# Kernel tuning notes

Measured on AMD Instinct MI355X. Metric: run time of the kernel, lower is better.

The kernel has to match this reference:

```python
import jax, jax.numpy as jnp
import numpy as np

B, Hn, Wn, C, NH, WS, SR = 4, 64, 64, 256, 8, 3, 8
HD = C // NH
N = Hn * Wn
L = WS * WS
PH, PW = Hn // SR, Wn // SR
P = PH * PW
T = 4096  # cpb table length
NEG = -1e30

def _l2norm(x, axis=-1):
    return x / jnp.maximum(jnp.linalg.norm(x, axis=axis, keepdims=True), 1e-12)

def _unfold(x, ws):
    # x: (B, C, H, W) -> (B, C, ws*ws, H*W), torch F.unfold channel ordering (C major)
    p = ws // 2
    b, c, h, w = x.shape
    xp = jnp.pad(x, ((0, 0), (0, 0), (p, p), (p, p)))
    pats = jnp.stack([xp[:, :, i:i + h, j:j + w] for i in range(ws) for j in range(ws)], axis=2)
    return pats.reshape(b, c, ws * ws, h * w)

def setup_inputs():
    key = jax.random.key(0)
    ks = jax.random.split(key, 16)
    def w(k, shape, s=0.02):
        return jax.random.normal(k, shape, jnp.float32) * s
    # buffers derived from the window geometry (get_seqlen_and_mask)
    ones = np.ones((Hn, Wn), np.float32)
    pad = WS // 2
    op = np.pad(ones, pad)
    pats = np.stack([op[i:i + Hn, j:j + Wn] for i in range(WS) for j in range(WS)], -1).reshape(N, L)
    padding_mask = jnp.asarray(pats == 0)
    seq_length_scale = jnp.asarray(np.log(pats.sum(-1, keepdims=True) + P).astype(np.float32))
    temperature = jnp.log(jnp.expm1(jnp.ones((NH, 1, 1), jnp.float32) / 0.24))
    return dict(
        x=jax.random.normal(ks[0], (B, N, C), jnp.float32),
        relative_pos_index=jax.random.randint(ks[1], (N, P), 0, T),
        relative_coords_table=jax.random.uniform(ks[2], (T, 2), jnp.float32, -1.0, 1.0),
        q_w=w(ks[3], (C, C)), q_b=jnp.zeros((C,), jnp.float32),
        kv_w=w(ks[4], (2 * C, C)), kv_b=jnp.zeros((2 * C,), jnp.float32),
        temperature=temperature,
        query_embedding=w(ks[5], (NH, 1, HD)),
        proj_w=w(ks[6], (C, C)), proj_b=jnp.zeros((C,), jnp.float32),
        sr_w=w(ks[7], (C, C)), sr_b=jnp.zeros((C,), jnp.float32),
        norm_g=jnp.ones((C,), jnp.float32), norm_b=jnp.zeros((C,), jnp.float32),
        cpb1_w=w(ks[8], (512, 2)), cpb1_b=jnp.zeros((512,), jnp.float32),
        cpb2_w=w(ks[9], (NH, 512)), cpb2_b=jnp.zeros((NH,), jnp.float32),
        rpb_local=w(ks[10], (NH, L), 0.0004),
        learnable_tokens=w(ks[11], (NH, HD, L)),
        learnable_bias=jnp.zeros((NH, 1, L), jnp.float32),
        seq_length_scale=seq_length_scale,
        padding_mask=padding_mask,
        H=Hn, W=Wn,
    )

def _forward(x, q_w, q_b, kv_w, kv_b, temperature, query_embedding, proj_w, proj_b,
             sr_w, sr_b, norm_g, norm_b, cpb1_w, cpb1_b, cpb2_w, cpb2_b, rpb_local,
             learnable_tokens, learnable_bias, seq_length_scale, relative_coords_table,
             relative_pos_index, padding_mask, H, W):
    b, n, c = x.shape
    # normalized queries, scaled by learnable temperature and log-seqlen
    q = (x @ q_w.T + q_b).reshape(b, n, NH, HD).transpose(0, 2, 1, 3)  # (B,h,N,d)
    q_norm = _l2norm(q)
    q_scaled = (q_norm + query_embedding[None]) * jax.nn.softplus(temperature)[None] * seq_length_scale
    # --- local branch: sliding-window QK with RPB ---
    kv = x @ kv_w.T + kv_b  # (B,N,2C)
    k_loc = _l2norm((kv[..., :c]).reshape(b, n, NH, HD)).reshape(b, n, c)
    kv_img = jnp.concatenate([k_loc, kv[..., c:]], -1).transpose(0, 2, 1).reshape(b, 2 * c, H, W)
    pats = _unfold(kv_img, WS).reshape(b, 2 * NH, HD, L, n).transpose(0, 1, 4, 2, 3)  # (B,2h,N,d,L)
    k_loc, v_loc = pats[:, :NH], pats[:, NH:]
    attn_local = jnp.einsum('bhnd,bhndl->bhnl', q_scaled, k_loc) + rpb_local[None, :, None, :]
    attn_local = jnp.where(padding_mask[None, None], NEG, attn_local)
    # --- pooled branch ---
    x_img = x.transpose(0, 2, 1).reshape(b, c, H, W)
    x_sr = jax.nn.gelu(jnp.einsum('bchw,oc->bohw', x_img, sr_w) + sr_b[None, :, None, None], approximate=False)
    x_pool = x_sr.reshape(b, c, PH, SR, PW, SR).mean((3, 5)).reshape(b, c, P).transpose(0, 2, 1)  # (B,P,C)
    mu = x_pool.mean(-1, keepdims=True)
    var = x_pool.var(-1, keepdims=True)
    x_pool = (x_pool - mu) / jnp.sqrt(var + 1e-5) * norm_g + norm_b
    kv_pool = (x_pool @ kv_w.T + kv_b).reshape(b, P, 2 * NH, HD).transpose(0, 2, 1, 3)
    k_pool, v_pool = kv_pool[:, :NH], kv_pool[:, NH:]  # (B,h,P,d)
    cpb = jax.nn.relu(relative_coords_table @ cpb1_w.T + cpb1_b) @ cpb2_w.T + cpb2_b  # (T,h)
    pool_bias = cpb.T[:, relative_pos_index.reshape(-1)].reshape(NH, n, P)
    attn_pool = jnp.einsum('bhnd,bhpd->bhnp', q_scaled, _l2norm(k_pool)) + pool_bias[None]
    # --- joint softmax over local + pooled keys ---
    attn = jax.nn.softmax(jnp.concatenate([attn_local, attn_pool], -1), axis=-1)
    attn_local, attn_pool = attn[..., :L], attn[..., L:]
    a = jnp.einsum('bhnd,hdl->bhnl', q_norm, learnable_tokens) + learnable_bias[None] + attn_local
    x_local = jnp.einsum('bhnl,bhndl->bhnd', a, v_loc)
    x_pool_out = jnp.einsum('bhnp,bhpd->bhnd', attn_pool, v_pool)
    out = (x_local + x_pool_out).transpose(0, 2, 1, 3).reshape(b, n, c)
    return out @ proj_w.T + proj_b

def reference(x, relative_pos_index, relative_coords_table, q_w, q_b, kv_w, kv_b, temperature,
              query_embedding, proj_w, proj_b, sr_w, sr_b, norm_g, norm_b, cpb1_w, cpb1_b,
              cpb2_w, cpb2_b, rpb_local, learnable_tokens, learnable_bias, seq_length_scale,
              padding_mask, H, W):
    return _forward(x, q_w, q_b, kv_w, kv_b, temperature, query_embedding, proj_w, proj_b,
                    sr_w, sr_b, norm_g, norm_b, cpb1_w, cpb1_b, cpb2_w, cpb2_b, rpb_local,
                    learnable_tokens, learnable_bias, seq_length_scale, relative_coords_table,
                    relative_pos_index, padding_mask, H, W)
```

## Files before the change

### kernel.cpp

```cpp
#include <hip/hip_runtime.h>
#include <hip/hip_bf16.h>

typedef unsigned short u16;
typedef unsigned int u32;

#define B_ 4
#define N_ 4096
#define C_ 256
#define NH_ 8
#define HD_ 32
#define L_ 9
#define P_ 64
#define T_ 4096
#define NEG_ (-1e30f)

typedef __attribute__((ext_vector_type(8))) short bf16x8;
typedef __attribute__((ext_vector_type(4))) float f32x4;

__device__ __forceinline__ float b2f(u16 u) {
    union { u32 i; float f; } v; v.i = ((u32)u) << 16; return v.f;
}
__device__ __forceinline__ u16 f2b(float f) {
    u32 x = __float_as_uint(f);
    u32 r = (x + 0x7fffu + ((x >> 16) & 1u)) >> 16;
    return (u16)r;
}
__device__ __forceinline__ short f2bs(float f) { return (short)f2b(f); }

__global__ __launch_bounds__(256) void prep_k(
    const float* __restrict__ x, const float* __restrict__ q_w, const float* __restrict__ kv_w,
    const float* __restrict__ sr_w, const float* __restrict__ proj_w,
    u16* __restrict__ xb, u16* __restrict__ wfused, u16* __restrict__ pwb,
    const float* __restrict__ table, const float* __restrict__ w1, const float* __restrict__ b1,
    const float* __restrict__ w2, const float* __restrict__ b2, float* __restrict__ cpb)
{
    __shared__ float w1s[512][2];
    __shared__ float b1s[512];
    __shared__ float w2s[8][512];
    int bid = blockIdx.x, tid = threadIdx.x;
    if (bid < 4096) {
        int i = bid * 256 + tid;
        float4 v = reinterpret_cast<const float4*>(x)[i];
        ushort4 o; o.x = f2b(v.x); o.y = f2b(v.y); o.z = f2b(v.z); o.w = f2b(v.w);
        reinterpret_cast<ushort4*>(xb)[i] = o;
    } else if (bid < 4416) {
        int i = (bid - 4096) * 256 + tid;
        const float* s; u16* d; int off;
        if (i < 16384)      { s = q_w;    d = wfused; off = i; }
        else if (i < 49152) { s = kv_w;   d = wfused; off = i; }
        else if (i < 65536) { s = sr_w;   d = wfused; off = i; }
        else                { s = proj_w; d = pwb;    off = i - 65536; }
        int soff = (i < 16384) ? i : (i < 49152) ? (i - 16384) : (i < 65536) ? (i - 49152) : (i - 65536);
        float4 v = reinterpret_cast<const float4*>(s)[soff];
        ushort4 o; o.x = f2b(v.x); o.y = f2b(v.y); o.z = f2b(v.z); o.w = f2b(v.w);
        reinterpret_cast<ushort4*>(d)[off] = o;
    } else {
        for (int i = tid; i < 512; i += 256) {
            w1s[i][0] = w1[i * 2]; w1s[i][1] = w1[i * 2 + 1]; b1s[i] = b1[i];
        }
        for (int i = tid; i < 4096; i += 256) w2s[i >> 9][i & 511] = w2[i];
        __syncthreads();
        int t = (bid - 4416) * 256 + tid;
        float t0 = table[t * 2], t1 = table[t * 2 + 1];
        float acc[8] = {};
        for (int j = 0; j < 512; ++j) {
            float h = fmaxf(t0 * w1s[j][0] + t1 * w1s[j][1] + b1s[j], 0.0f);
            #pragma unroll
            for (int hh = 0; hh < 8; ++hh) acc[hh] += h * w2s[hh][j];
        }
        #pragma unroll
        for (int hh = 0; hh < 8; ++hh) cpb[t * 8 + hh] = acc[hh] + b2[hh];
    }
}

template<int MODE>
__global__ __launch_bounds__(256) void gemm_big_k(
    const u16* __restrict__ A, const u16* __restrict__ W,
    const float* __restrict__ b0, const float* __restrict__ b1, const float* __restrict__ b2,
    float* __restrict__ qn, float* __restrict__ kv, u16* __restrict__ xgb, float* __restrict__ pout)
{
    const int K = 256;
    int tid = threadIdx.x, w = tid >> 6, lane = tid & 63;
    int quad = lane >> 4, l16 = lane & 15;
    int wr = w >> 1, wc = w & 1;
    int rowBase = blockIdx.y * 128 + wr * 64;
    int colBase = blockIdx.x * 128 + wc * 64;
    f32x4 acc[4][4] = {};
    const u16* aptr = A + (size_t)(rowBase + l16) * K + quad * 8;
    const u16* wptr = W + (size_t)(colBase + l16) * K + quad * 8;
    for (int k0 = 0; k0 < K; k0 += 32) {
        bf16x8 af[4], bfr[4];
        #pragma unroll
        for (int i = 0; i < 4; ++i) af[i] = *reinterpret_cast<const bf16x8*>(aptr + (size_t)i * 16 * K + k0);
        #pragma unroll
        for (int j = 0; j < 4; ++j) bfr[j] = *reinterpret_cast<const bf16x8*>(wptr + (size_t)j * 16 * K + k0);
        #pragma unroll
        for (int i = 0; i < 4; ++i)
            #pragma unroll
            for (int j = 0; j < 4; ++j)
                acc[i][j] = __builtin_amdgcn_mfma_f32_16x16x32_bf16(af[i], bfr[j], acc[i][j], 0, 0, 0);
    }
    int rng = (MODE == 0) ? (colBase >> 8) : 99;
    float bj[4];
    #pragma unroll
    for (int j = 0; j < 4; ++j) {
        int gc = colBase + j * 16 + l16;
        if (MODE == 1)      bj[j] = b0[gc];
        else if (rng == 0)  bj[j] = b0[gc];
        else if (rng <= 2)  bj[j] = b1[gc - 256];
        else                bj[j] = b2[gc - 768];
    }
    #pragma unroll
    for (int i = 0; i < 4; ++i) {
        float vals[4][4];
        #pragma unroll
        for (int j = 0; j < 4; ++j)
            #pragma unroll
            for (int r = 0; r < 4; ++r) {
                float t = acc[i][j][r] + bj[j];
                if (MODE == 0 && rng == 3) t = 0.5f * t * (1.0f + erff(t * 0.70710678118654752f));
                vals[j][r] = t;
            }
        if (MODE == 0 && rng <= 1) {
            #pragma unroll
            for (int hp = 0; hp < 2; ++hp)
                #pragma unroll
                for (int r = 0; r < 4; ++r) {
                    float s = vals[2*hp][r] * vals[2*hp][r] + vals[2*hp+1][r] * vals[2*hp+1][r];
                    s += __shfl_xor(s, 1); s += __shfl_xor(s, 2);
                    s += __shfl_xor(s, 4); s += __shfl_xor(s, 8);
                    float inv = 1.0f / fmaxf(sqrtf(s), 1e-12f);
                    vals[2*hp][r] *= inv; vals[2*hp+1][r] *= inv;
                }
        }
        #pragma unroll
        for (int j = 0; j < 4; ++j) {
            int gc = colBase + j * 16 + l16;
            #pragma unroll
            for (int r = 0; r < 4; ++r) {
                int row = rowBase + i * 16 + quad * 4 + r;
                if (MODE == 1)      pout[(size_t)row * 256 + gc] = vals[j][r];
                else if (rng == 0)  qn[(size_t)row * 256 + gc] = vals[j][r];
                else if (rng <= 2)  kv[(size_t)row * 512 + gc - 256] = vals[j][r];
                else                xgb[(size_t)row * 256 + gc - 768] = f2b(vals[j][r]);
            }
        }
    }
}

__global__ __launch_bounds__(256) void poolkv_k(
    const u16* __restrict__ xgb, const float* __restrict__ g, const float* __restrict__ bta,
    const float* __restrict__ kv_w, const float* __restrict__ kv_b, float* __restrict__ kvp)
{
    __shared__ __align__(16) float xps[256];
    __shared__ float r1[4], r2[4];
    int bp = blockIdx.x;
    int b = bp >> 6, p = bp & 63;
    int py = p >> 3, px = p & 7;
    int o = threadIdx.x;
    float s = 0.0f;
    for (int sy = 0; sy < 8; ++sy)
        #pragma unroll
        for (int sx = 0; sx < 8; ++sx) {
            int pix = (py * 8 + sy) * 64 + px * 8 + sx;
            s += b2f(xgb[((size_t)(b * N_ + pix)) * C_ + o]);
        }
    float v = s * (1.0f / 64.0f);
    float s1 = v, s2 = v * v;
    #pragma unroll
    for (int off = 32; off >= 1; off >>= 1) { s1 += __shfl_xor(s1, off); s2 += __shfl_xor(s2, off); }
    int wv = o >> 6, ln = o & 63;
    if (ln == 0) { r1[wv] = s1; r2[wv] = s2; }
    __syncthreads();
    float S1 = r1[0] + r1[1] + r1[2] + r1[3];
    float S2 = r2[0] + r2[1] + r2[2] + r2[3];
    float mu = S1 * (1.0f / 256.0f);
    float var = S2 * (1.0f / 256.0f) - mu * mu;
    xps[o] = (v - mu) * rsqrtf(var + 1e-5f) * g[o] + bta[o];
    __syncthreads();
    float a0 = kv_b[o], a1 = kv_b[o + 256];
    const float4* xp4 = (const float4*)xps;
    const float4* w0 = (const float4*)(kv_w + (size_t)o * 256);
    const float4* w1 = (const float4*)(kv_w + (size_t)(o + 256) * 256);
    #pragma unroll 4
    for (int k4 = 0; k4 < 64; ++k4) {
        float4 xv = xp4[k4]; float4 wa = w0[k4]; float4 wb = w1[k4];
        a0 += xv.x * wa.x + xv.y * wa.y + xv.z * wa.z + xv.w * wa.w;
        a1 += xv.x * wb.x + xv.y * wb.y + xv.z * wb.z + xv.w * wb.w;
    }
    float ss = a0 * a0;
    ss += __shfl_xor(ss, 1); ss += __shfl_xor(ss, 2); ss += __shfl_xor(ss, 4);
    ss += __shfl_xor(ss, 8); ss += __shfl_xor(ss, 16);
    a0 *= 1.0f / fmaxf(sqrtf(ss), 1e-12f);
    kvp[(size_t)bp * 512 + o] = a0;
    kvp[(size_t)bp * 512 + 256 + o] = a1;
}

__global__ __launch_bounds__(256) void attn_k(
    const float* __restrict__ qn, const float* __restrict__ kv,
    const float* __restrict__ kvp, const float* __restrict__ cpb,
    const int* __restrict__ rpi, const float* __restrict__ temp,
    const float* __restrict__ qe, const float* __restrict__ lt,
    const float* __restrict__ rpb, const float* __restrict__ lb,
    const float* __restrict__ slsin, u16* __restrict__ aob)
{
    __shared__ u16 kp_hi[64 * 40], kp_lo[64 * 40];
    __shared__ u16 vp_hi[32 * 72], vp_lo[32 * 72];
    __shared__ u16 ltb[16 * 32];
    __shared__ float qs_w[4][16][36];
    __shared__ float S_w[4][16][88];
    __shared__ float rpb_s[9], lb_s[9];

    int bid = blockIdx.x;
    int tile = bid & 63, h = (bid >> 6) & 7, b = bid >> 9;
    int tid = threadIdx.x, wave = tid >> 6, lane = tid & 63;
    int quad = lane >> 4, l16 = lane & 15;

    {
        int p = tid >> 2, dc = (tid & 3) * 8;
        const float* src = kvp + ((size_t)(b * P_ + p)) * 512 + h * 32 + dc;
        float4 k0 = *(const float4*)(src), k1 = *(const float4*)(src + 4);
        float4 v0 = *(const float4*)(src + 256), v1 = *(const float4*)(src + 260);
        float kf[8] = {k0.x,k0.y,k0.z,k0.w,k1.x,k1.y,k1.z,k1.w};
        float vf[8] = {v0.x,v0.y,v0.z,v0.w,v1.x,v1.y,v1.z,v1.w};
        #pragma unroll
        for (int j = 0; j < 8; ++j) {
            u16 khi = f2b(kf[j]);
            kp_hi[p * 40 + dc + j] = khi;
            kp_lo[p * 40 + dc + j] = f2b(kf[j] - b2f(khi));
            u16 vhi = f2b(vf[j]);
            vp_hi[(dc + j) * 72 + p] = vhi;
            vp_lo[(dc + j) * 72 + p] = f2b(vf[j] - b2f(vhi));
        }
    }
    for (int t = tid; t < 512; t += 256) {
        int l = t & 15, d = t >> 4;
        ltb[l * 32 + d] = (l < 9) ? f2b(lt[h * 288 + d * 9 + l]) : (u16)0;
    }
    if (tid < 9) { rpb_s[tid] = rpb[h * 9 + tid]; lb_s[tid] = lb[h * 9 + tid]; }
    __syncthreads();

    int n0w = tile * 64 + wave * 16;
    float tsc = log1pf(expf(temp[h]));
    bf16x8 qs_hi, qs_lo, qn_b;
    {
        int n = n0w + l16;
        const float* qptr = qn + ((size_t)(b * N_ + n)) * C_ + h * 32 + quad * 8;
        float4 q0 = *(const float4*)qptr, q1 = *(const float4*)(qptr + 4);
        const float* qeptr = qe + h * 32 + quad * 8;
        float4 e0 = *(const float4*)qeptr, e1 = *(const float4*)(qeptr + 4);
        float slv = slsin[n];
        float qf[8] = {q0.x,q0.y,q0.z,q0.w,q1.x,q1.y,q1.z,q1.w};
        float ef[8] = {e0.x,e0.y,e0.z,e0.w,e1.x,e1.y,e1.z,e1.w};
        #pragma unroll
        for (int j = 0; j < 8; ++j) {
            float qs = (qf[j] + ef[j]) * tsc * slv;
            u16 hi = f2b(qs);
            qs_hi[j] = (short)hi;
            qs_lo[j] = f2bs(qs - b2f(hi));
            qn_b[j]  = f2bs(qf[j]);
            qs_w[wave][l16][quad * 8 + j] = qs;
        }
        if (quad == 0) { S_w[wave][l16][73] = NEG_; S_w[wave][l16][74] = NEG_; S_w[wave][l16][75] = NEG_; }
    }

    #pragma unroll
    for (int jt = 0; jt < 4; ++jt) {
        bf16x8 bh = *(const bf16x8*)&kp_hi[(jt * 16 + l16) * 40 + quad * 8];
        bf16x8 bl = *(const bf16x8*)&kp_lo[(jt * 16 + l16) * 40 + quad * 8];
        f32x4 a = {};
        a = __builtin_amdgcn_mfma_f32_16x16x32_bf16(qs_lo, bh, a, 0, 0, 0);
        a = __builtin_amdgcn_mfma_f32_16x16x32_bf16(qs_hi, bl, a, 0, 0, 0);
        a = __builtin_amdgcn_mfma_f32_16x16x32_bf16(qs_hi, bh, a, 0, 0, 0);
        #pragma unroll
        for (int r = 0; r < 4; ++r) {
            int pix = quad * 4 + r;
            int n = n0w + pix;
            int idx = rpi[n * P_ + jt * 16 + l16];
            S_w[wave][pix][jt * 16 + l16] = a[r] + cpb[(size_t)idx * 8 + h];
        }
    }
    f32x4 accL;
    {
        bf16x8 ltf = *(const bf16x8*)&ltb[l16 * 32 + quad * 8];
        f32x4 z = {};
        accL = __builtin_amdgcn_mfma_f32_16x16x32_bf16(qn_b, ltf, z, 0, 0, 0);
    }
    for (int t = lane; t < 144; t += 64) {
        int pix = t / 9, l = t - pix * 9;
        int n = n0w + pix, y = n >> 6, x = n & 63;
        int ny = y + l / 3 - 1, nx = x + (l % 3) - 1;
        bool ok = ((unsigned)ny < 64u) && ((unsigned)nx < 64u);
        int nn = ok ? ny * 64 + nx : n;
        const float4* kb = (const float4*)(kv + ((size_t)(b * N_ + nn)) * 512 + h * 32);
        float acl = 0.0f;
        #pragma unroll
        for (int d4 = 0; d4 < 8; ++d4) {
            float4 kk = kb[d4];
            float4 qq = *(const float4*)&qs_w[wave][pix][d4 * 4];
            acl += qq.x * kk.x + qq.y * kk.y + qq.z * kk.z + qq.w * kk.w;
        }
        S_w[wave][pix][64 + l] = ok ? (acl + rpb_s[l]) : NEG_;
    }
    {
        int pix = lane >> 2, c0 = (lane & 3) * 19;
        float vals[19]; float mx = NEG_;
        #pragma unroll
        for (int i = 0; i < 19; ++i) { vals[i] = S_w[wave][pix][c0 + i]; mx = fmaxf(mx, vals[i]); }
        mx = fmaxf(mx, __shfl_xor(mx, 1));
        mx = fmaxf(mx, __shfl_xor(mx, 2));
        float sm = 0.0f;
        #pragma unroll
        for (int i = 0; i < 19; ++i) { vals[i] = expf(vals[i] - mx); sm += vals[i]; }
        sm += __shfl_xor(sm, 1); sm += __shfl_xor(sm, 2);
        float inv = 1.0f / sm;
        #pragma unroll
        for (int i = 0; i < 19; ++i) S_w[wave][pix][c0 + i] = vals[i] * inv;
    }
    if (l16 < 9) {
        #pragma unroll
        for (int r = 0; r < 4; ++r) {
            int pix = quad * 4 + r;
            int n = n0w + pix, y = n >> 6, x = n & 63;
            int ny = y + l16 / 3 - 1, nx = x + (l16 % 3) - 1;
            bool ok = ((unsigned)ny < 64u) && ((unsigned)nx < 64u);
            S_w[wave][pix][76 + l16] = ok ? (accL[r] + lb_s[l16] + S_w[wave][pix][64 + l16]) : 0.0f;
        }
    }
    f32x4 accO[2] = {};
    #pragma unroll
    for (int kc = 0; kc < 2; ++kc) {
        float wf[8];
        *(float4*)&wf[0] = *(const float4*)&S_w[wave][l16][kc * 32 + quad * 8];
        *(float4*)&wf[4] = *(const float4*)&S_w[wave][l16][kc * 32 + quad * 8 + 4];
        bf16x8 w_hi, w_lo;
        #pragma unroll
        for (int j = 0; j < 8; ++j) {
            u16 hi = f2b(wf[j]);
            w_hi[j] = (short)hi;
            w_lo[j] = f2bs(wf[j] - b2f(hi));
        }
        #pragma unroll
        for (int nt = 0; nt < 2; ++nt) {
            bf16x8 vh = *(const bf16x8*)&vp_hi[(nt * 16 + l16) * 72 + kc * 32 + quad * 8];
            bf16x8 vl = *(const bf16x8*)&vp_lo[(nt * 16 + l16) * 72 + kc * 32 + quad * 8];
            accO[nt] = __builtin_amdgcn_mfma_f32_16x16x32_bf16(w_lo, vh, accO[nt], 0, 0, 0);
            accO[nt] = __builtin_amdgcn_mfma_f32_16x16x32_bf16(w_hi, vl, accO[nt], 0, 0, 0);
            accO[nt] = __builtin_amdgcn_mfma_f32_16x16x32_bf16(w_hi, vh, accO[nt], 0, 0, 0);
        }
    }
    #pragma unroll
    for (int r = 0; r < 4; ++r) {
        int pix = quad * 4 + r;
        int n = n0w + pix, y = n >> 6, x = n & 63;
        #pragma unroll
        for (int l = 0; l < 9; ++l) {
            int ny = y + l / 3 - 1, nx = x + (l % 3) - 1;
            bool ok = ((unsigned)ny < 64u) && ((unsigned)nx < 64u);
            int nn = ok ? ny * 64 + nx : n;
            float aw = S_w[wave][pix][76 + l];
            const float* vb = kv + ((size_t)(b * N_ + nn)) * 512 + 256 + h * 32;
            accO[0][r] += aw * vb[l16];
            accO[1][r] += aw * vb[16 + l16];
        }
    }
    #pragma unroll
    for (int nt = 0; nt < 2; ++nt)
        #pragma unroll
        for (int r = 0; r < 4; ++r) {
            int n = n0w + quad * 4 + r;
            aob[((size_t)(b * N_ + n)) * C_ + h * 32 + nt * 16 + l16] = f2b(accO[nt][r]);
        }
}

extern "C" void kernel_launch(void* const* d_in, const int* in_sizes, int n_in,
                              void* d_out, int out_size, void* d_ws, size_t ws_size,
                              hipStream_t stream) {
    const float* x      = (const float*)d_in[0];
    const int*   rpi    = (const int*)d_in[1];
    const float* table  = (const float*)d_in[2];
    const float* q_w    = (const float*)d_in[3];
    const float* q_b    = (const float*)d_in[4];
    const float* kv_w   = (const float*)d_in[5];
    const float* kv_b   = (const float*)d_in[6];
    const float* temp   = (const float*)d_in[7];
    const float* qe     = (const float*)d_in[8];
    const float* proj_w = (const float*)d_in[9];
    const float* proj_b = (const float*)d_in[10];
    const float* sr_w   = (const float*)d_in[11];
    const float* sr_b   = (const float*)d_in[12];
    const float* norm_g = (const float*)d_in[13];
    const float* norm_b = (const float*)d_in[14];
    const float* cpb1_w = (const float*)d_in[15];
    const float* cpb1_b = (const float*)d_in[16];
    const float* cpb2_w = (const float*)d_in[17];
    const float* cpb2_b = (const float*)d_in[18];
    const float* rpb    = (const float*)d_in[19];
    const float* lt     = (const float*)d_in[20];
    const float* lb     = (const float*)d_in[21];
    const float* sls    = (const float*)d_in[22];

    float* ws  = (float*)d_ws;
    float* qn  = ws;
    float* kv  = qn  + (size_t)B_ * N_ * C_;
    float* kvp = kv  + (size_t)B_ * N_ * 2 * C_;
    float* cpb = kvp + (size_t)B_ * P_ * 2 * C_;
    u16*   xb  = (u16*)(cpb + (size_t)T_ * NH_);
    u16*   wfb = xb  + (size_t)B_ * N_ * C_;
    u16*   pwb = wfb + (size_t)1024 * C_;
    u16*   xgb = pwb + (size_t)C_ * C_;
    u16*   aob = xgb;

    dim3 blk(256);

    prep_k<<<dim3(4432), blk, 0, stream>>>(x, q_w, kv_w, sr_w, proj_w, xb, wfb, pwb,
                                           table, cpb1_w, cpb1_b, cpb2_w, cpb2_b, cpb);
    gemm_big_k<0><<<dim3(8, 128), blk, 0, stream>>>(xb, wfb, q_b, kv_b, sr_b, qn, kv, xgb, nullptr);
    poolkv_k<<<dim3(B_ * P_), blk, 0, stream>>>(xgb, norm_g, norm_b, kv_w, kv_b, kvp);
    attn_k<<<dim3(B_ * NH_ * 64), blk, 0, stream>>>(qn, kv, kvp, cpb, rpi, temp, qe, lt, rpb, lb, sls, aob);
    gemm_big_k<1><<<dim3(2, 128), blk, 0, stream>>>(aob, pwb, proj_b, nullptr, nullptr,
                                                    nullptr, nullptr, nullptr, (float*)d_out);
}
```

Baseline: 293.9 us.

## Stage weight tiles in LDS for GEMMs, split pooled KV projection across blocks

The GEMM kernel now loads a 64-column slab of the full-K weight matrix into shared memory once per block. Each wave computes RI×4 MFMA tiles against that slab, with 64 columns per block and a grid reshaped to 16×64 and 4×256. The pooled KV kernel doubles its block count so each block computes only K or only V, which halves the per-thread dot-product work. The attention kernel moves its local weights to a separate small shared array and hoists the temperature computation ahead of the barrier. The GEMM change trades some A-matrix register reuse and more blocks for less global weight traffic.

New measurement: 277.4 us. 1.06x faster.

```diff
diff --git a/kernel.cpp b/kernel.cpp
--- a/kernel.cpp
+++ b/kernel.cpp
@@ -79,26 +79,35 @@
     const float* __restrict__ b0, const float* __restrict__ b1, const float* __restrict__ b2,
     float* __restrict__ qn, float* __restrict__ kv, u16* __restrict__ xgb, float* __restrict__ pout)
 {
-    const int K = 256;
+    constexpr int RI = (MODE == 0) ? 4 : 1;
+    __shared__ u16 Bs[64 * 264];
     int tid = threadIdx.x, w = tid >> 6, lane = tid & 63;
     int quad = lane >> 4, l16 = lane & 15;
-    int wr = w >> 1, wc = w & 1;
-    int rowBase = blockIdx.y * 128 + wr * 64;
-    int colBase = blockIdx.x * 128 + wc * 64;
-    f32x4 acc[4][4] = {};
-    const u16* aptr = A + (size_t)(rowBase + l16) * K + quad * 8;
-    const u16* wptr = W + (size_t)(colBase + l16) * K + quad * 8;
-    for (int k0 = 0; k0 < K; k0 += 32) {
-        bf16x8 af[4], bfr[4];
-        #pragma unroll
-        for (int i = 0; i < 4; ++i) af[i] = *reinterpret_cast<const bf16x8*>(aptr + (size_t)i * 16 * K + k0);
-        #pragma unroll
-        for (int j = 0; j < 4; ++j) bfr[j] = *reinterpret_cast<const bf16x8*>(wptr + (size_t)j * 16 * K + k0);
-        #pragma unroll
-        for (int i = 0; i < 4; ++i)
+    int colBase = blockIdx.x * 64;
+    #pragma unroll
+    for (int c = 0; c < 8; ++c) {
+        int linear = c * 256 + tid;
+        int col = linear >> 5, kc = linear & 31;
+        uint4 v = *reinterpret_cast<const uint4*>(W + (size_t)(colBase + col) * 256 + kc * 8);
+        *reinterpret_cast<uint4*>(&Bs[col * 264 + kc * 8]) = v;
+    }
+    __syncthreads();
+    int rowBase = blockIdx.y * (RI * 64) + w * (RI * 16);
+    f32x4 acc[RI][4] = {};
+    const u16* aptr = A + (size_t)(rowBase + l16) * 256 + quad * 8;
+    #pragma unroll
+    for (int k0 = 0; k0 < 256; k0 += 32) {
+        bf16x8 af[RI];
+        #pragma unroll
+        for (int i = 0; i < RI; ++i)
+            af[i] = *reinterpret_cast<const bf16x8*>(aptr + (size_t)i * 16 * 256 + k0);
+        #pragma unroll
+        for (int j = 0; j < 4; ++j) {
+            bf16x8 bfr = *reinterpret_cast<const bf16x8*>(&Bs[(j * 16 + l16) * 264 + k0 + quad * 8]);
             #pragma unroll
-            for (int j = 0; j < 4; ++j)
-                acc[i][j] = __builtin_amdgcn_mfma_f32_16x16x32_bf16(af[i], bfr[j], acc[i][j], 0, 0, 0);
+            for (int i = 0; i < RI; ++i)
+                acc[i][j] = __builtin_amdgcn_mfma_f32_16x16x32_bf16(af[i], bfr, acc[i][j], 0, 0, 0);
+        }
     }
     int rng = (MODE == 0) ? (colBase >> 8) : 99;
     float bj[4];
@@ -111,7 +120,7 @@
         else                bj[j] = b2[gc - 768];
     }
     #pragma unroll
-    for (int i = 0; i < 4; ++i) {
+    for (int i = 0; i < RI; ++i) {
         float vals[4][4];
         #pragma unroll
         for (int j = 0; j < 4; ++j)
@@ -154,7 +163,8 @@
 {
     __shared__ __align__(16) float xps[256];
     __shared__ float r1[4], r2[4];
-    int bp = blockIdx.x;
+    int bid = blockIdx.x;
+    int bp = bid >> 1, half = bid & 1;
     int b = bp >> 6, p = bp & 63;
     int py = p >> 3, px = p & 7;
     int o = threadIdx.x;
@@ -178,22 +188,22 @@
     float var = S2 * (1.0f / 256.0f) - mu * mu;
     xps[o] = (v - mu) * rsqrtf(var + 1e-5f) * g[o] + bta[o];
     __syncthreads();
-    float a0 = kv_b[o], a1 = kv_b[o + 256];
+    int col = half * 256 + o;
+    float a = kv_b[col];
     const float4* xp4 = (const float4*)xps;
-    const float4* w0 = (const float4*)(kv_w + (size_t)o * 256);
-    const float4* w1 = (const float4*)(kv_w + (size_t)(o + 256) * 256);
-    #pragma unroll 4
+    const float4* wrow = (const float4*)(kv_w + (size_t)col * 256);
+    #pragma unroll 8
     for (int k4 = 0; k4 < 64; ++k4) {
-        float4 xv = xp4[k4]; float4 wa = w0[k4]; float4 wb = w1[k4];
-        a0 += xv.x * wa.x + xv.y * wa.y + xv.z * wa.z + xv.w * wa.w;
-        a1 += xv.x * wb.x + xv.y * wb.y + xv.z * wb.z + xv.w * wb.w;
-    }
-    float ss = a0 * a0;
-    ss += __shfl_xor(ss, 1); ss += __shfl_xor(ss, 2); ss += __shfl_xor(ss, 4);
-    ss += __shfl_xor(ss, 8); ss += __shfl_xor(ss, 16);
-    a0 *= 1.0f / fmaxf(sqrtf(ss), 1e-12f);
-    kvp[(size_t)bp * 512 + o] = a0;
-    kvp[(size_t)bp * 512 + 256 + o] = a1;
+        float4 xv = xp4[k4]; float4 wa = wrow[k4];
+        a += xv.x * wa.x + xv.y * wa.y + xv.z * wa.z + xv.w * wa.w;
+    }
+    if (half == 0) {
+        float ss = a * a;
+        ss += __shfl_xor(ss, 1); ss += __shfl_xor(ss, 2); ss += __shfl_xor(ss, 4);
+        ss += __shfl_xor(ss, 8); ss += __shfl_xor(ss, 16);
+        a *= 1.0f / fmaxf(sqrtf(ss), 1e-12f);
+    }
+    kvp[(size_t)bp * 512 + col] = a;
 }
 
 __global__ __launch_bounds__(256) void attn_k(
@@ -208,7 +218,8 @@
     __shared__ u16 vp_hi[32 * 72], vp_lo[32 * 72];
     __shared__ u16 ltb[16 * 32];
     __shared__ float qs_w[4][16][36];
-    __shared__ float S_w[4][16][88];
+    __shared__ float S_w[4][16][76];
+    __shared__ float aw_s[4][16][12];
     __shared__ float rpb_s[9], lb_s[9];
 
     int bid = blockIdx.x;
@@ -238,10 +249,10 @@
         ltb[l * 32 + d] = (l < 9) ? f2b(lt[h * 288 + d * 9 + l]) : (u16)0;
     }
     if (tid < 9) { rpb_s[tid] = rpb[h * 9 + tid]; lb_s[tid] = lb[h * 9 + tid]; }
+    float tsc = log1pf(expf(temp[h]));
     __syncthreads();
 
     int n0w = tile * 64 + wave * 16;
-    float tsc = log1pf(expf(temp[h]));
     bf16x8 qs_hi, qs_lo, qn_b;
     {
         int n = n0w + l16;
@@ -324,7 +335,7 @@
             int n = n0w + pix, y = n >> 6, x = n & 63;
             int ny = y + l16 / 3 - 1, nx = x + (l16 % 3) - 1;
             bool ok = ((unsigned)ny < 64u) && ((unsigned)nx < 64u);
-            S_w[wave][pix][76 + l16] = ok ? (accL[r] + lb_s[l16] + S_w[wave][pix][64 + l16]) : 0.0f;
+            aw_s[wave][pix][l16] = ok ? (accL[r] + lb_s[l16] + S_w[wave][pix][64 + l16]) : 0.0f;
         }
     }
     f32x4 accO[2] = {};
@@ -358,7 +369,7 @@
             int ny = y + l / 3 - 1, nx = x + (l % 3) - 1;
             bool ok = ((unsigned)ny < 64u) && ((unsigned)nx < 64u);
             int nn = ok ? ny * 64 + nx : n;
-            float aw = S_w[wave][pix][76 + l];
+            float aw = aw_s[wave][pix][l];
             const float* vb = kv + ((size_t)(b * N_ + nn)) * 512 + 256 + h * 32;
             accO[0][r] += aw * vb[l16];
             accO[1][r] += aw * vb[16 + l16];
@@ -415,9 +426,9 @@
 
     prep_k<<<dim3(4432), blk, 0, stream>>>(x, q_w, kv_w, sr_w, proj_w, xb, wfb, pwb,
                                            table, cpb1_w, cpb1_b, cpb2_w, cpb2_b, cpb);
-    gemm_big_k<0><<<dim3(8, 128), blk, 0, stream>>>(xb, wfb, q_b, kv_b, sr_b, qn, kv, xgb, nullptr);
-    poolkv_k<<<dim3(B_ * P_), blk, 0, stream>>>(xgb, norm_g, norm_b, kv_w, kv_b, kvp);
+    gemm_big_k<0><<<dim3(16, 64), blk, 0, stream>>>(xb, wfb, q_b, kv_b, sr_b, qn, kv, xgb, nullptr);
+    poolkv_k<<<dim3(B_ * P_ * 2), blk, 0, stream>>>(xgb, norm_g, norm_b, kv_w, kv_b, kvp);
     attn_k<<<dim3(B_ * NH_ * 64), blk, 0, stream>>>(qn, kv, kvp, cpb, rpi, temp, qe, lt, rpb, lb, sls, aob);
-    gemm_big_k<1><<<dim3(2, 128), blk, 0, stream>>>(aob, pwb, proj_b, nullptr, nullptr,
+    gemm_big_k<1><<<dim3(4, 256), blk, 0, stream>>>(aob, pwb, proj_b, nullptr, nullptr,
                                                     nullptr, nullptr, nullptr, (float*)d_out);
 }
```
